# Performance work log

Hardware: AMD Instinct MI355X
Metric: run time of the kernel (lower is better)

The kernel has to match this reference:

```python
import jax, jax.numpy as jnp
import numpy as np

B, C, D, N, NCLS = 2048, 96, 384, 200000, 10
LN_EPS = 1e-5


def setup_inputs() -> dict:
    key = jax.random.key(0)
    ks = jax.random.split(key, 16)
    s = 0.05  # keep squared-distance logits in a sane range
    inp = {
        'k': jax.random.normal(ks[0], (B, D), jnp.float32) * s,
        'context_idx': jax.random.randint(ks[1], (B, C), 0, N),
        'candidate_embeddings': jax.random.normal(ks[2], (N, D), jnp.float32) * s,
        'candidate_y': jax.random.randint(ks[3], (N,), 0, NCLS),
        # learned params
        'label_emb': jax.random.normal(ks[4], (NCLS, D), jnp.float32) * 0.02,
        'ln_g': jnp.ones((D,), jnp.float32),
        'ln_b': jnp.zeros((D,), jnp.float32),
        'kp_w1': jax.random.normal(ks[5], (D, D), jnp.float32) * (1.0 / np.sqrt(D)),
        'kp_b1': jnp.zeros((D,), jnp.float32),
        'kp_w2': jax.random.normal(ks[6], (D, D), jnp.float32) * (1.0 / np.sqrt(D)),
        'kp_b2': jnp.zeros((D,), jnp.float32),
        'pw1': jax.random.normal(ks[7], (D, D), jnp.float32) * (1.0 / np.sqrt(D)),
        'pb1': jnp.zeros((D,), jnp.float32),
        'pw2': jax.random.normal(ks[8], (D, NCLS), jnp.float32) * (1.0 / np.sqrt(D)),
        'pb2': jnp.zeros((NCLS,), jnp.float32),
    }
    return inp


def reference(k, context_idx, candidate_embeddings, candidate_y,
              label_emb, ln_g, ln_b, kp_w1, kp_b1, kp_w2, kp_b2,
              pw1, pb1, pw2, pb2):
    # gather context (irregular access): [B, C, D], [B, C]
    context_k = candidate_embeddings[context_idx]
    context_y = candidate_y[context_idx]

    # negative squared distance via kernel trick: -|k|^2 + 2 k.ck - |ck|^2
    sim = (-jnp.sum(k * k, axis=-1, keepdims=True)
           + 2.0 * jnp.einsum('bd,bcd->bc', k, context_k)
           - jnp.sum(context_k * context_k, axis=-1))  # [B, C]
    probs = jax.nn.softmax(sim, axis=-1)  # dropout is identity in eval mode

    context_y_emb = label_emb[context_y]  # [B, C, D]

    # key_proj: LayerNorm -> Linear -> SiLU -> Linear, residual (d_main==n_out)
    def key_proj(x):
        mu = jnp.mean(x, axis=-1, keepdims=True)
        var = jnp.mean(jnp.square(x - mu), axis=-1, keepdims=True)
        h = (x - mu) * jax.lax.rsqrt(var + LN_EPS) * ln_g + ln_b
        h = jax.nn.silu(h @ kp_w1 + kp_b1)
        h = h @ kp_w2 + kp_b2
        return x + h

    # Abl == -1 branch: values = label_emb + key_proj(k - context_k)
    values = context_y_emb + key_proj(k[:, None, :] - context_k)  # [B, C, D]

    # probs[:, None] @ values -> weighted sum over context
    context_x = jnp.einsum('bc,bcd->bd', probs, values)
    x = k + context_x

    # predictor MLP (no residual: d_main != n_classes)
    h = jax.nn.silu(x @ pw1 + pb1)
    y = h @ pw2 + pb2
    return y
```

## Files before the change

### kernel.cpp

```cpp
#include <hip/hip_runtime.h>
#include <hip/hip_bf16.h>

#define BB   2048
#define CC   96
#define DD   384
#define NCLSS 10
#define AS_STRIDE 392

typedef __attribute__((ext_vector_type(8))) __bf16 bf16x8;
typedef __attribute__((ext_vector_type(4))) float  floatx4;
typedef unsigned int  uint32;
typedef unsigned short ushort16;
typedef __attribute__((ext_vector_type(4))) uint32 uintx4;

__device__ __forceinline__ float bflo(uint32 u){ return __uint_as_float(u << 16); }
__device__ __forceinline__ float bfhi(uint32 u){ return __uint_as_float(u & 0xffff0000u); }
__device__ __forceinline__ float bf1(ushort16 s){ return __uint_as_float(((uint32)s) << 16); }
__device__ __forceinline__ ushort16 f2bf(float f){
  uint32 u = __float_as_uint(f);
  return (ushort16)((u + 0x7fffu + ((u >> 16) & 1u)) >> 16);
}
__device__ __forceinline__ int probe_f32(const void* lng_raw){
  return (((const uint32*)lng_raw)[0] == 0x3F800000u) ? 1 : 0;
}
__device__ __forceinline__ float ld1(const void* p, size_t i, int isf32){
  return isf32 ? ((const float*)p)[i] : bf1(((const ushort16*)p)[i]);
}
__device__ __forceinline__ void ld8(const void* base, size_t eoff, int isf32, float v[8]){
  if (isf32){
    const floatx4* p = (const floatx4*)((const float*)base + eoff);
    floatx4 a = p[0], b = p[1];
    v[0]=a[0]; v[1]=a[1]; v[2]=a[2]; v[3]=a[3];
    v[4]=b[0]; v[5]=b[1]; v[6]=b[2]; v[7]=b[3];
  } else {
    uintx4 a = *(const uintx4*)((const ushort16*)base + eoff);
    v[0]=bflo(a[0]); v[1]=bfhi(a[0]); v[2]=bflo(a[1]); v[3]=bfhi(a[1]);
    v[4]=bflo(a[2]); v[5]=bfhi(a[2]); v[6]=bflo(a[3]); v[7]=bfhi(a[3]);
  }
}

__global__ __launch_bounds__(256) void k_canon(
    const void* w1, const void* w2, const void* pw1, const void* lng,
    ushort16* __restrict__ wW1T, ushort16* __restrict__ wW2T,
    ushort16* __restrict__ wPW1T)
{
  int isf32 = probe_f32(lng);
  int m  = blockIdx.x / 144;
  int t  = blockIdx.x % 144;
  int tr = t / 12, tc = t % 12;
  const void* src = (m == 0) ? w1 : (m == 1) ? w2 : pw1;
  ushort16* dst   = (m == 0) ? wW1T : (m == 1) ? wW2T : wPW1T;
  __shared__ float tile[32][33];
  int tx = threadIdx.x & 31, ty = threadIdx.x >> 5;
  #pragma unroll
  for (int p = 0; p < 4; p++)
    tile[p*8 + ty][tx] = ld1(src, (size_t)(tr*32 + p*8 + ty) * DD + tc*32 + tx, isf32);
  __syncthreads();
  float gmul = (m == 0) ? ld1(lng, tr*32 + tx, isf32) : 1.f;
  #pragma unroll
  for (int p = 0; p < 4; p++)
    dst[(size_t)(tc*32 + p*8 + ty) * DD + tr*32 + tx] = f2bf(tile[tx][p*8 + ty] * gmul);
}

__global__ __launch_bounds__(384) void k_vec(
    const void* w1, const void* lng, const void* lnb, const void* b1,
    float* __restrict__ sconst, float* __restrict__ tconst)
{
  int isf32 = probe_f32(lng);
  int n = threadIdx.x;
  float s = 0.f, tt = 0.f;
  for (int j = 0; j < DD; j++) {
    float w = ld1(w1, (size_t)j * DD + n, isf32);
    s  += ld1(lng, j, isf32) * w;
    tt += ld1(lnb, j, isf32) * w;
  }
  sconst[n] = s;
  tconst[n] = tt + ld1(b1, n, isf32);
}

__global__ __launch_bounds__(512, 4) void k_fused(
    const void* kptr, const int* __restrict__ cidx,
    const void* cand, const int* __restrict__ cy,
    const void* lng,
    const ushort16* __restrict__ w1t,
    const float* __restrict__ sconst, const float* __restrict__ tconst,
    float* __restrict__ wxpre, float* __restrict__ wpl, float* __restrict__ wsum)
{
  int isf32 = probe_f32(lng);
  int b = blockIdx.x;
  int tid = threadIdx.x, wave = tid >> 6, lane = tid & 63;
  int t = lane & 15, kq = lane >> 4;
  __shared__ __align__(16) char AsB[96 * 768];
  __shared__ float sims[CC], probs[CC], rsigv[CC], rmuv[CC];
  __shared__ float plbuf[NCLSS], xacc[DD];

  if (tid < NCLSS) plbuf[tid] = 0.f;
  if (tid < DD)    xacc[tid]  = 0.f;

  int tr_ = (t < 12) ? t : t - 12;
  int c  = wave * 12 + tr_;
  int idx = cidx[b * CC + c];
  int swz = (c & 7) << 4;

  float s1 = 0.f, s2 = 0.f;
  #pragma unroll 2
  for (int kt = 0; kt < 12; kt++) {
    int j0 = kt * 32 + kq * 8;
    float ck[8], kk[8];
    ld8(cand, (size_t)idx * DD + j0, isf32, ck);
    ld8(kptr, (size_t)b   * DD + j0, isf32, kk);
    uint32 w[4];
    #pragma unroll
    for (int p = 0; p < 4; p++) {
      float d0 = kk[2*p]   - ck[2*p];
      float d1 = kk[2*p+1] - ck[2*p+1];
      s1 += d0 + d1; s2 += d0*d0 + d1*d1;
      w[p] = (uint32)f2bf(d0) | ((uint32)f2bf(d1) << 16);
    }
    if (t < 12) {
      uintx4 vv = { w[0], w[1], w[2], w[3] };
      *(uintx4*)(AsB + ((c * 768 + kt * 64 + kq * 16) ^ swz)) = vv;
    }
  }
  s1 += __shfl_xor(s1, 16); s2 += __shfl_xor(s2, 16);
  s1 += __shfl_xor(s1, 32); s2 += __shfl_xor(s2, 32);
  float mu = s1 * (1.f/DD), var = s2 * (1.f/DD) - mu*mu;
  float rsig = rsqrtf(var + 1e-5f);
  if (kq == 0 && t < 12) { sims[c] = -s2; rsigv[c] = rsig; rmuv[c] = rsig * mu; }
  __syncthreads();

  if (wave == 0) {
    float v0 = sims[lane];
    float v1 = (lane < 32) ? sims[lane + 64] : -1e30f;
    float mx = fmaxf(v0, v1);
    #pragma unroll
    for (int m = 32; m; m >>= 1) mx = fmaxf(mx, __shfl_xor(mx, m));
    float e0 = __expf(v0 - mx);
    float e1 = (lane < 32) ? __expf(v1 - mx) : 0.f;
    float s = e0 + e1;
    #pragma unroll
    for (int m = 32; m; m >>= 1) s += __shfl_xor(s, m);
    float inv = 1.f / s;
    probs[lane] = e0 * inv;
    if (lane < 32) probs[lane + 64] = e1 * inv;
  }
  __syncthreads();

  if (tid < CC) atomicAdd(&plbuf[cy[cidx[b * CC + tid]]], probs[tid]);
  {
    float T0=0,T1=0,T2=0,T3=0,T4=0,T5=0;
    #pragma unroll
    for (int i = 0; i < 12; i++) {
      int cc = wave * 12 + i;
      float p = probs[cc];
      const char* rp = AsB + cc * 768;
      int sz = (cc & 7) << 4;
      uint32 a0 = *(const uint32*)(rp + ((lane*12 + 0) ^ sz));
      uint32 a1 = *(const uint32*)(rp + ((lane*12 + 4) ^ sz));
      uint32 a2 = *(const uint32*)(rp + ((lane*12 + 8) ^ sz));
      T0 += p*bflo(a0); T1 += p*bfhi(a0); T2 += p*bflo(a1);
      T3 += p*bfhi(a1); T4 += p*bflo(a2); T5 += p*bfhi(a2);
    }
    int j0 = lane * 6;
    atomicAdd(&xacc[j0+0], T0); atomicAdd(&xacc[j0+1], T1);
    atomicAdd(&xacc[j0+2], T2); atomicAdd(&xacc[j0+3], T3);
    atomicAdd(&xacc[j0+4], T4); atomicAdd(&xacc[j0+5], T5);
  }
  __syncthreads();

  if (tid < DD)
    wxpre[(size_t)b * DD + tid] = ld1(kptr, (size_t)b * DD + tid, isf32) + xacc[tid];
  if (tid < NCLSS) wpl[b * NCLSS + tid] = plbuf[tid];

  int col = lane & 15, quad = lane >> 4;
  int n0 = wave * 48;
  floatx4 acc[6][3];
  #pragma unroll
  for (int i = 0; i < 6; i++)
    #pragma unroll
    for (int j = 0; j < 3; j++) acc[i][j] = (floatx4)0.f;

  const ushort16* wbase = w1t + (size_t)(n0 + col) * DD + quad * 8;
  bf16x8 bcur[3];
  #pragma unroll
  for (int tn = 0; tn < 3; tn++)
    bcur[tn] = *(const bf16x8*)(wbase + (size_t)tn * 16 * DD);
  #pragma unroll 1
  for (int kt = 0; kt < 12; kt++) {
    bf16x8 bnxt[3] = { (bf16x8)0, (bf16x8)0, (bf16x8)0 };
    if (kt < 11) {
      #pragma unroll
      for (int tn = 0; tn < 3; tn++)
        bnxt[tn] = *(const bf16x8*)(wbase + (size_t)tn * 16 * DD + (kt+1) * 32);
    }
    #pragma unroll
    for (int tm = 0; tm < 6; tm++) {
      int r = tm*16 + col;
      bf16x8 afrag = *(const bf16x8*)(AsB + ((r * 768 + kt*64 + quad*16) ^ ((r & 7) << 4)));
      #pragma unroll
      for (int tn = 0; tn < 3; tn++)
        acc[tm][tn] = __builtin_amdgcn_mfma_f32_16x16x32_bf16(afrag, bcur[tn], acc[tm][tn], 0, 0, 0);
    }
    #pragma unroll
    for (int tn = 0; tn < 3; tn++) bcur[tn] = bnxt[tn];
  }

  #pragma unroll
  for (int tn = 0; tn < 3; tn++) {
    int n = n0 + tn*16 + col;
    float sn = sconst[n], tnc = tconst[n];
    float val = 0.f;
    #pragma unroll
    for (int tm = 0; tm < 6; tm++) {
      #pragma unroll
      for (int r = 0; r < 4; r++) {
        int row = tm*16 + quad*4 + r;
        float h = rsigv[row] * acc[tm][tn][r] - rmuv[row] * sn + tnc;
        h = h / (1.f + __expf(-h));
        val += probs[row] * h;
      }
    }
    val += __shfl_xor(val, 16);
    val += __shfl_xor(val, 32);
    if (quad == 0) wsum[(size_t)b * DD + n] = val;
  }
}

__global__ __launch_bounds__(512) void k_final(
    const float* __restrict__ wxpre, const float* __restrict__ wsum,
    const float* __restrict__ wpl, const void* lemb,
    const ushort16* __restrict__ w2t, const void* b2,
    const ushort16* __restrict__ pw1t, const void* pb1,
    const void* pw2, const void* pb2,
    const void* lng_raw, void* out)
{
  int isf32 = probe_f32(lng_raw);
  int b0 = blockIdx.x * 8;
  int tid = threadIdx.x, wave = tid >> 6, lane = tid & 63;
  int cn = lane & 15, quad = lane >> 4;
  __shared__ __align__(16) ushort16 As[16 * AS_STRIDE];
  __shared__ float hbuf[8][AS_STRIDE];
  __shared__ float lembsh[NCLSS * DD];
  __shared__ float plsh[8][NCLSS];
  __shared__ float part[480];

  for (int e = tid; e < 16 * AS_STRIDE; e += 512) {
    int r = e / AS_STRIDE, j = e - r * AS_STRIDE;
    ushort16 v = (ushort16)0;
    if (r < 8 && j < DD) v = f2bf(wsum[(size_t)(b0 + r) * DD + j]);
    As[e] = v;
  }
  for (int e = tid; e < NCLSS * DD; e += 512) lembsh[e] = ld1(lemb, e, isf32);
  if (tid < 80) plsh[tid / NCLSS][tid % NCLSS] = wpl[(b0 + tid / NCLSS) * NCLSS + tid % NCLSS];
  __syncthreads();

  int n0 = wave * 48;
  floatx4 acc[3];
  #pragma unroll
  for (int j = 0; j < 3; j++) acc[j] = (floatx4)0.f;
  const ushort16* wb2 = w2t + (size_t)(n0 + cn) * DD + quad * 8;
  #pragma unroll 2
  for (int kt = 0; kt < 12; kt++) {
    bf16x8 afrag = *(const bf16x8*)(As + cn * AS_STRIDE + kt*32 + quad*8);
    #pragma unroll
    for (int tn = 0; tn < 3; tn++) {
      bf16x8 bfrag = *(const bf16x8*)(wb2 + (size_t)tn * 16 * DD + kt * 32);
      acc[tn] = __builtin_amdgcn_mfma_f32_16x16x32_bf16(afrag, bfrag, acc[tn], 0, 0, 0);
    }
  }
  float xv[3][4];
  #pragma unroll
  for (int tn = 0; tn < 3; tn++) {
    int n = n0 + tn*16 + cn;
    float bb = ld1(b2, n, isf32);
    #pragma unroll
    for (int r = 0; r < 4; r++) {
      int row = quad*4 + r;
      if (row < 8) {
        float v = acc[tn][r] + bb + wxpre[(size_t)(b0 + row) * DD + n];
        #pragma unroll
        for (int l = 0; l < NCLSS; l++) v += plsh[row][l] * lembsh[l * DD + n];
        xv[tn][r] = v;
      }
    }
  }
  __syncthreads();
  #pragma unroll
  for (int tn = 0; tn < 3; tn++) {
    int n = n0 + tn*16 + cn;
    #pragma unroll
    for (int r = 0; r < 4; r++) {
      int row = quad*4 + r;
      if (row < 8) As[row * AS_STRIDE + n] = f2bf(xv[tn][r]);
    }
  }
  __syncthreads();

  floatx4 acc2[3];
  #pragma unroll
  for (int j = 0; j < 3; j++) acc2[j] = (floatx4)0.f;
  const ushort16* wbp = pw1t + (size_t)(n0 + cn) * DD + quad * 8;
  #pragma unroll 2
  for (int kt = 0; kt < 12; kt++) {
    bf16x8 afrag = *(const bf16x8*)(As + cn * AS_STRIDE + kt*32 + quad*8);
    #pragma unroll
    for (int tn = 0; tn < 3; tn++) {
      bf16x8 bfrag = *(const bf16x8*)(wbp + (size_t)tn * 16 * DD + kt * 32);
      acc2[tn] = __builtin_amdgcn_mfma_f32_16x16x32_bf16(afrag, bfrag, acc2[tn], 0, 0, 0);
    }
  }
  #pragma unroll
  for (int tn = 0; tn < 3; tn++) {
    int n = n0 + tn*16 + cn;
    float bb = ld1(pb1, n, isf32);
    #pragma unroll
    for (int r = 0; r < 4; r++) {
      int row = quad*4 + r;
      if (row < 8) {
        float h = acc2[tn][r] + bb;
        hbuf[row][n] = h / (1.f + __expf(-h));
      }
    }
  }
  __syncthreads();

  if (tid < 480) {
    int r = tid / 60, rem = tid % 60, n = rem / 6, s = rem % 6;
    float pp = 0.f;
    int jb = s * 64;
    #pragma unroll 8
    for (int jj = 0; jj < 64; jj++) {
      int j = jb + jj;
      pp += hbuf[r][j] * ld1(pw2, (size_t)j * NCLSS + n, isf32);
    }
    part[tid] = pp;
  }
  __syncthreads();
  if (tid < 80) {
    int r = tid / NCLSS, n = tid % NCLSS;
    float y = ld1(pb2, n, isf32);
    #pragma unroll
    for (int s = 0; s < 6; s++) y += part[r*60 + n*6 + s];
    size_t o = (size_t)(b0 + r) * NCLSS + n;
    if (isf32) ((float*)out)[o] = y;
    else       ((ushort16*)out)[o] = f2bf(y);
  }
}

extern "C" void kernel_launch(void* const* d_in, const int* in_sizes, int n_in,
                              void* d_out, int out_size, void* d_ws, size_t ws_size,
                              hipStream_t stream) {
  const void* kptr = d_in[0];
  const int*  cidx = (const int*)d_in[1];
  const void* cand = d_in[2];
  const int*  cy   = (const int*)d_in[3];
  const void* lemb = d_in[4];
  const void* lng  = d_in[5];
  const void* lnb  = d_in[6];
  const void* w1   = d_in[7];
  const void* b1   = d_in[8];
  const void* w2   = d_in[9];
  const void* b2   = d_in[10];
  const void* pw1  = d_in[11];
  const void* pb1  = d_in[12];
  const void* pw2  = d_in[13];
  const void* pb2  = d_in[14];

  char* ws = (char*)d_ws;
  ushort16* wW1T   = (ushort16*)(ws);
  ushort16* wW2T   = (ushort16*)(ws + 294912);
  ushort16* wPW1T  = (ushort16*)(ws + 589824);
  float*    wxpre  = (float*)   (ws + 884736);
  float*    wpl    = (float*)   (ws + 4030464);
  float*    wsum   = (float*)   (ws + 4112384);
  float*    sconst = (float*)   (ws + 7258112);
  float*    tconst = (float*)   (ws + 7259648);

  k_vec<<<1, 384, 0, stream>>>(w1, lng, lnb, b1, sconst, tconst);
  k_canon<<<432, 256, 0, stream>>>(w1, w2, pw1, lng, wW1T, wW2T, wPW1T);
  k_fused<<<BB, 512, 0, stream>>>(kptr, cidx, cand, cy, lng, wW1T,
                                  sconst, tconst, wxpre, wpl, wsum);
  k_final<<<256, 512, 0, stream>>>(wxpre, wsum, wpl, lemb, wW2T, b2,
                                   wPW1T, pb1, pw2, pb2, lng, d_out);
}
```

Baseline: 709.9 us.

## Fold k_vec into k_canon, stage k in LDS, batch candidate gather loads

Removes the single-block k_vec launch. Its column reductions now run as 12 extra blocks of k_canon, with an 8-way split and a shared-memory reduce, so they overlap with the transpose work. In k_fused the query row k is loaded once into LDS, not re-read from global for every context row, and the candidate-row gather issues all (or half) of its vector loads up front so more memory requests are in flight. This costs more registers per thread and adds a __syncthreads, which could lower occupancy in a kernel already bounded to 4 blocks of 512.

```diff
diff --git a/kernel.cpp b/kernel.cpp
--- a/kernel.cpp
+++ b/kernel.cpp
@@ -26,25 +26,36 @@
 __device__ __forceinline__ float ld1(const void* p, size_t i, int isf32){
   return isf32 ? ((const float*)p)[i] : bf1(((const ushort16*)p)[i]);
 }
-__device__ __forceinline__ void ld8(const void* base, size_t eoff, int isf32, float v[8]){
-  if (isf32){
-    const floatx4* p = (const floatx4*)((const float*)base + eoff);
-    floatx4 a = p[0], b = p[1];
-    v[0]=a[0]; v[1]=a[1]; v[2]=a[2]; v[3]=a[3];
-    v[4]=b[0]; v[5]=b[1]; v[6]=b[2]; v[7]=b[3];
-  } else {
-    uintx4 a = *(const uintx4*)((const ushort16*)base + eoff);
-    v[0]=bflo(a[0]); v[1]=bfhi(a[0]); v[2]=bflo(a[1]); v[3]=bfhi(a[1]);
-    v[4]=bflo(a[2]); v[5]=bfhi(a[2]); v[6]=bflo(a[3]); v[7]=bfhi(a[3]);
-  }
-}
 
 __global__ __launch_bounds__(256) void k_canon(
-    const void* w1, const void* w2, const void* pw1, const void* lng,
+    const void* w1, const void* w2, const void* pw1,
+    const void* lng, const void* lnb, const void* b1,
     ushort16* __restrict__ wW1T, ushort16* __restrict__ wW2T,
-    ushort16* __restrict__ wPW1T)
+    ushort16* __restrict__ wPW1T,
+    float* __restrict__ sconst, float* __restrict__ tconst)
 {
   int isf32 = probe_f32(lng);
+  if (blockIdx.x >= 432) {
+    __shared__ float sred[8][32], tred[8][32];
+    int bid = blockIdx.x - 432;
+    int nl = threadIdx.x & 31, jl = threadIdx.x >> 5;
+    int n = bid * 32 + nl;
+    float s = 0.f, tt = 0.f;
+    for (int j = jl; j < DD; j += 8) {
+      float w = ld1(w1, (size_t)j * DD + n, isf32);
+      s  += ld1(lng, j, isf32) * w;
+      tt += ld1(lnb, j, isf32) * w;
+    }
+    sred[jl][nl] = s; tred[jl][nl] = tt;
+    __syncthreads();
+    if (jl == 0) {
+      #pragma unroll
+      for (int r = 1; r < 8; r++) { s += sred[r][nl]; tt += tred[r][nl]; }
+      sconst[n] = s;
+      tconst[n] = tt + ld1(b1, n, isf32);
+    }
+    return;
+  }
   int m  = blockIdx.x / 144;
   int t  = blockIdx.x % 144;
   int tr = t / 12, tc = t % 12;
@@ -60,22 +71,6 @@
   #pragma unroll
   for (int p = 0; p < 4; p++)
     dst[(size_t)(tc*32 + p*8 + ty) * DD + tr*32 + tx] = f2bf(tile[tx][p*8 + ty] * gmul);
-}
-
-__global__ __launch_bounds__(384) void k_vec(
-    const void* w1, const void* lng, const void* lnb, const void* b1,
-    float* __restrict__ sconst, float* __restrict__ tconst)
-{
-  int isf32 = probe_f32(lng);
-  int n = threadIdx.x;
-  float s = 0.f, tt = 0.f;
-  for (int j = 0; j < DD; j++) {
-    float w = ld1(w1, (size_t)j * DD + n, isf32);
-    s  += ld1(lng, j, isf32) * w;
-    tt += ld1(lnb, j, isf32) * w;
-  }
-  sconst[n] = s;
-  tconst[n] = tt + ld1(b1, n, isf32);
 }
 
 __global__ __launch_bounds__(512, 4) void k_fused(
@@ -91,35 +86,82 @@
   int tid = threadIdx.x, wave = tid >> 6, lane = tid & 63;
   int t = lane & 15, kq = lane >> 4;
   __shared__ __align__(16) char AsB[96 * 768];
+  __shared__ __align__(16) float ksh[DD];
   __shared__ float sims[CC], probs[CC], rsigv[CC], rmuv[CC];
   __shared__ float plbuf[NCLSS], xacc[DD];
 
   if (tid < NCLSS) plbuf[tid] = 0.f;
-  if (tid < DD)    xacc[tid]  = 0.f;
+  if (tid < DD) {
+    xacc[tid] = 0.f;
+    ksh[tid]  = ld1(kptr, (size_t)b * DD + tid, isf32);
+  }
 
   int tr_ = (t < 12) ? t : t - 12;
   int c  = wave * 12 + tr_;
   int idx = cidx[b * CC + c];
   int swz = (c & 7) << 4;
+  __syncthreads();
 
   float s1 = 0.f, s2 = 0.f;
-  #pragma unroll 2
-  for (int kt = 0; kt < 12; kt++) {
-    int j0 = kt * 32 + kq * 8;
-    float ck[8], kk[8];
-    ld8(cand, (size_t)idx * DD + j0, isf32, ck);
-    ld8(kptr, (size_t)b   * DD + j0, isf32, kk);
-    uint32 w[4];
-    #pragma unroll
-    for (int p = 0; p < 4; p++) {
-      float d0 = kk[2*p]   - ck[2*p];
-      float d1 = kk[2*p+1] - ck[2*p+1];
-      s1 += d0 + d1; s2 += d0*d0 + d1*d1;
-      w[p] = (uint32)f2bf(d0) | ((uint32)f2bf(d1) << 16);
-    }
-    if (t < 12) {
-      uintx4 vv = { w[0], w[1], w[2], w[3] };
-      *(uintx4*)(AsB + ((c * 768 + kt * 64 + kq * 16) ^ swz)) = vv;
+  if (!isf32) {
+    const uintx4* cp = (const uintx4*)((const ushort16*)cand + (size_t)idx * DD);
+    uintx4 ckr[12];
+    #pragma unroll
+    for (int kt = 0; kt < 12; kt++) ckr[kt] = cp[kt*4 + kq];
+    #pragma unroll
+    for (int kt = 0; kt < 12; kt++) {
+      int j0 = kt*32 + kq*8;
+      floatx4 ka = *(const floatx4*)&ksh[j0];
+      floatx4 kb = *(const floatx4*)&ksh[j0+4];
+      float kk[8] = {ka[0],ka[1],ka[2],ka[3],kb[0],kb[1],kb[2],kb[3]};
+      float ck[8] = {bflo(ckr[kt][0]),bfhi(ckr[kt][0]),bflo(ckr[kt][1]),bfhi(ckr[kt][1]),
+                     bflo(ckr[kt][2]),bfhi(ckr[kt][2]),bflo(ckr[kt][3]),bfhi(ckr[kt][3])};
+      uint32 w[4];
+      #pragma unroll
+      for (int p = 0; p < 4; p++) {
+        float d0 = kk[2*p]   - ck[2*p];
+        float d1 = kk[2*p+1] - ck[2*p+1];
+        s1 += d0 + d1; s2 += d0*d0 + d1*d1;
+        w[p] = (uint32)f2bf(d0) | ((uint32)f2bf(d1) << 16);
+      }
+      if (t < 12) {
+        uintx4 vv = { w[0], w[1], w[2], w[3] };
+        *(uintx4*)(AsB + ((c * 768 + kt * 64 + kq * 16) ^ swz)) = vv;
+      }
+    }
+  } else {
+    const float* cf = (const float*)cand + (size_t)idx * DD;
+    #pragma unroll
+    for (int h = 0; h < 2; h++) {
+      floatx4 cr[12];
+      #pragma unroll
+      for (int q = 0; q < 6; q++) {
+        int j0 = (h*6+q)*32 + kq*8;
+        cr[2*q]   = *(const floatx4*)(cf + j0);
+        cr[2*q+1] = *(const floatx4*)(cf + j0 + 4);
+      }
+      #pragma unroll
+      for (int q = 0; q < 6; q++) {
+        int kt = h*6 + q;
+        int j0 = kt*32 + kq*8;
+        floatx4 ka = *(const floatx4*)&ksh[j0];
+        floatx4 kb = *(const floatx4*)&ksh[j0+4];
+        float kk[8] = {ka[0],ka[1],ka[2],ka[3],kb[0],kb[1],kb[2],kb[3]};
+        float ck[8] = {cr[2*q][0],cr[2*q][1],cr[2*q][2],cr[2*q][3],
+                       cr[2*q+1][0],cr[2*q+1][1],cr[2*q+1][2],cr[2*q+1][3]};
+        uint32 w[4];
+        #pragma unroll
+        for (int p = 0; p < 4; p++) {
+          float d0 = kk[2*p]   - ck[2*p];
+          float d1 = kk[2*p+1] - ck[2*p+1];
+          s1 += d0 + d1; s2 += d0*d0 + d1*d1;
+          w[p] = (uint32)f2bf(d0) | ((uint32)f2bf(d1) << 16);
+        }
+        if (t < 12) {
+          uintx4 vv = { w[0], w[1], w[2], w[3] };
+          *(uintx4*)(AsB + ((c * 768 + kt * 64 + kq * 16) ^ swz)) = vv;
+        }
+      }
     }
   }
   s1 += __shfl_xor(s1, 16); s2 += __shfl_xor(s2, 16);
@@ -169,7 +211,7 @@
   __syncthreads();
 
   if (tid < DD)
-    wxpre[(size_t)b * DD + tid] = ld1(kptr, (size_t)b * DD + tid, isf32) + xacc[tid];
+    wxpre[(size_t)b * DD + tid] = ksh[tid] + xacc[tid];
   if (tid < NCLSS) wpl[b * NCLSS + tid] = plbuf[tid];
 
   int col = lane & 15, quad = lane >> 4;
@@ -376,8 +418,8 @@
   float*    sconst = (float*)   (ws + 7258112);
   float*    tconst = (float*)   (ws + 7259648);
 
-  k_vec<<<1, 384, 0, stream>>>(w1, lng, lnb, b1, sconst, tconst);
-  k_canon<<<432, 256, 0, stream>>>(w1, w2, pw1, lng, wW1T, wW2T, wPW1T);
+  k_canon<<<444, 256, 0, stream>>>(w1, w2, pw1, lng, lnb, b1,
+                                   wW1T, wW2T, wPW1T, sconst, tconst);
   k_fused<<<BB, 512, 0, stream>>>(kptr, cidx, cand, cy, lng, wW1T,
                                   sconst, tconst, wxpre, wpl, wsum);
   k_final<<<256, 512, 0, stream>>>(wxpre, wsum, wpl, lemb, wW2T, b2,
```

After: 574.5 us. -19.1%, faster.
